# Kernel optimization log

Hardware: AMD Instinct MI355X
Metric: run time of the kernel (lower is better)

The kernel has to match this reference:

```python
import math
import jax, jax.numpy as jnp
import numpy as np

EMB = 1024
HEADS = 16
EXPAND = 2
HEAD_D = EMB // HEADS * EXPAND  # 128
N, S = 2, 2048


def setup_inputs() -> dict:
    key = jax.random.key(0)
    ks = jax.random.split(key, 10)
    lim = 1.0 / math.sqrt(EMB)  # nn.Linear default init range
    inp = {
        "query": jax.random.normal(ks[0], (N, S, EMB), dtype=jnp.float32),
        "key": jax.random.normal(ks[1], (N, S, EMB), dtype=jnp.float32),
        "value": jax.random.normal(ks[2], (N, S, EMB), dtype=jnp.float32),
        "mask": jax.random.randint(ks[3], (1, S, S), 0, 2, dtype=jnp.int32),
        "Wq": jax.random.uniform(ks[4], (EMB * EXPAND, EMB), jnp.float32, -lim, lim),
        "bq": jax.random.uniform(ks[5], (EMB * EXPAND,), jnp.float32, -lim, lim),
        "Wk": jax.random.uniform(ks[6], (EMB * EXPAND, EMB), jnp.float32, -lim, lim),
        "bk": jax.random.uniform(ks[7], (EMB * EXPAND,), jnp.float32, -lim, lim),
        "Wv": jax.random.uniform(ks[8], (EMB * EXPAND, EMB), jnp.float32, -lim, lim),
        "bv": jax.random.uniform(ks[9], (EMB * EXPAND,), jnp.float32, -lim, lim),
    }
    return inp


def _split_heads(x):
    # (N, S, H*D) -> (N, H, S, D)
    n, s, _ = x.shape
    return x.reshape(n, s, HEADS, HEAD_D).transpose(0, 2, 1, 3)


def reference(query, key, value, mask, Wq, bq, Wk, bk, Wv, bv):
    Q = _split_heads(jax.nn.relu(query @ Wq.T + bq))  # (N,H,S,D)
    K = _split_heads(jax.nn.relu(key @ Wk.T + bk))
    V = _split_heads(jax.nn.relu(value @ Wv.T + bv))
    scale = 1.0 / math.sqrt(HEAD_D)
    scores = jnp.einsum("nhqd,nhkd->nhqk", Q, K) * scale  # (N,H,S,S)
    scores = jnp.where(mask[None, :, :, :] == 0, jnp.float32(-1e7), scores)
    probs = jax.nn.softmax(scores, axis=-1)
    y = jnp.einsum("nhqk,nhkd->nhqd", probs, V)  # (N,H,S,D)
    return y.transpose(0, 2, 1, 3).reshape(query.shape[0], S, HEADS * HEAD_D)
```

## Files before the change

### kernel.cpp

```cpp
#include <hip/hip_runtime.h>

typedef __bf16 bf16;
typedef __bf16 bf16x8 __attribute__((ext_vector_type(8)));
typedef __bf16 bf16x4 __attribute__((ext_vector_type(4)));
typedef float f32x4 __attribute__((ext_vector_type(4)));

#define MFMA_BF16(A, B, C) __builtin_amdgcn_mfma_f32_16x16x32_bf16((A), (B), (C), 0, 0, 0)

#define EMB 1024
#define ODIM 2048
#define SEQ 2048
#define HEADS 16
#define HD 128

__global__ __launch_bounds__(256) void build_maskbits_k(const int* __restrict__ mask,
                                                        unsigned long long* __restrict__ mb) {
  int w = blockIdx.x * 256 + threadIdx.x;
  int q = w >> 5, c = w & 31;
  const int4* m4 = reinterpret_cast<const int4*>(mask + (size_t)q * SEQ + c * 64);
  unsigned long long bits = 0ull;
#pragma unroll
  for (int i = 0; i < 16; ++i) {
    int4 v = m4[i];
    if (v.x) bits |= 1ull << (i * 4 + 0);
    if (v.y) bits |= 1ull << (i * 4 + 1);
    if (v.z) bits |= 1ull << (i * 4 + 2);
    if (v.w) bits |= 1ull << (i * 4 + 3);
  }
  mb[w] = bits;
}

__global__ __launch_bounds__(256) void proj_gemm_k(const float* __restrict__ X,
                                                   const float* __restrict__ W,
                                                   const float* __restrict__ bias,
                                                   bf16* __restrict__ outN,
                                                   bf16* __restrict__ outT,
                                                   int vmode, float oscale) {
  __shared__ union {
    struct { bf16 A[128][40]; bf16 B[128][40]; } s;
    bf16 C[128][136];
  } sm;

  const int t = threadIdx.x;
  const int lane = t & 63;
  const int wid = t >> 6;
  const int wm = wid >> 1, wn = wid & 1;
  const int lr = lane & 15, lg = lane >> 4;
  const int m0 = blockIdx.y * 128;
  const int n0 = blockIdx.x * 128;
  const int sr = t >> 1, sh = (t & 1) * 16;

  const f32x4 fzero = {0.f, 0.f, 0.f, 0.f};
  f32x4 acc[4][4];
#pragma unroll
  for (int i = 0; i < 4; ++i)
#pragma unroll
    for (int j = 0; j < 4; ++j) acc[i][j] = fzero;

  const float* Xr = X + (size_t)(m0 + sr) * EMB + sh;
  const float* Wr = W + (size_t)(n0 + sr) * EMB + sh;

  float4 ar[4], br[4];
  {
    const float4* pa = reinterpret_cast<const float4*>(Xr);
    const float4* pb = reinterpret_cast<const float4*>(Wr);
#pragma unroll
    for (int i = 0; i < 4; ++i) { ar[i] = pa[i]; br[i] = pb[i]; }
  }

  for (int k0 = 0; k0 < EMB; k0 += 32) {
    {
      bf16x8 v0, v1, w0, w1;
      v0[0] = (bf16)ar[0].x; v0[1] = (bf16)ar[0].y; v0[2] = (bf16)ar[0].z; v0[3] = (bf16)ar[0].w;
      v0[4] = (bf16)ar[1].x; v0[5] = (bf16)ar[1].y; v0[6] = (bf16)ar[1].z; v0[7] = (bf16)ar[1].w;
      v1[0] = (bf16)ar[2].x; v1[1] = (bf16)ar[2].y; v1[2] = (bf16)ar[2].z; v1[3] = (bf16)ar[2].w;
      v1[4] = (bf16)ar[3].x; v1[5] = (bf16)ar[3].y; v1[6] = (bf16)ar[3].z; v1[7] = (bf16)ar[3].w;
      w0[0] = (bf16)br[0].x; w0[1] = (bf16)br[0].y; w0[2] = (bf16)br[0].z; w0[3] = (bf16)br[0].w;
      w0[4] = (bf16)br[1].x; w0[5] = (bf16)br[1].y; w0[6] = (bf16)br[1].z; w0[7] = (bf16)br[1].w;
      w1[0] = (bf16)br[2].x; w1[1] = (bf16)br[2].y; w1[2] = (bf16)br[2].z; w1[3] = (bf16)br[2].w;
      w1[4] = (bf16)br[3].x; w1[5] = (bf16)br[3].y; w1[6] = (bf16)br[3].z; w1[7] = (bf16)br[3].w;
      *(bf16x8*)&sm.s.A[sr][sh] = v0;
      *(bf16x8*)&sm.s.A[sr][sh + 8] = v1;
      *(bf16x8*)&sm.s.B[sr][sh] = w0;
      *(bf16x8*)&sm.s.B[sr][sh + 8] = w1;
    }
    __syncthreads();
    if (k0 + 32 < EMB) {
      const float4* pa = reinterpret_cast<const float4*>(Xr + k0 + 32);
      const float4* pb = reinterpret_cast<const float4*>(Wr + k0 + 32);
#pragma unroll
      for (int i = 0; i < 4; ++i) { ar[i] = pa[i]; br[i] = pb[i]; }
    }
    bf16x8 af[4], bfr[4];
#pragma unroll
    for (int i = 0; i < 4; ++i) af[i] = *(const bf16x8*)&sm.s.A[wm * 64 + i * 16 + lr][lg * 8];
#pragma unroll
    for (int i = 0; i < 4; ++i) bfr[i] = *(const bf16x8*)&sm.s.B[wn * 64 + i * 16 + lr][lg * 8];
#pragma unroll
    for (int mi = 0; mi < 4; ++mi)
#pragma unroll
      for (int ni = 0; ni < 4; ++ni)
        acc[mi][ni] = MFMA_BF16(af[mi], bfr[ni], acc[mi][ni]);
    __syncthreads();
  }

  float bv_[4];
#pragma unroll
  for (int ni = 0; ni < 4; ++ni) bv_[ni] = bias[n0 + wn * 64 + ni * 16 + lr];

  if (!vmode) {
#pragma unroll
    for (int mi = 0; mi < 4; ++mi)
#pragma unroll
      for (int ni = 0; ni < 4; ++ni)
#pragma unroll
        for (int j = 0; j < 4; ++j) {
          float v = fmaxf(acc[mi][ni][j] + bv_[ni], 0.f) * oscale;
          int row = m0 + wm * 64 + mi * 16 + lg * 4 + j;
          int col = n0 + wn * 64 + ni * 16 + lr;
          outN[(size_t)row * ODIM + col] = (bf16)v;
        }
  } else {
#pragma unroll
    for (int mi = 0; mi < 4; ++mi)
#pragma unroll
      for (int ni = 0; ni < 4; ++ni)
#pragma unroll
        for (int j = 0; j < 4; ++j) {
          float v = fmaxf(acc[mi][ni][j] + bv_[ni], 0.f) * oscale;
          int rit = wm * 64 + mi * 16 + lg * 4 + j;
          int cit = wn * 64 + ni * 16 + lr;
          sm.C[cit][rit] = (bf16)v;
        }
    __syncthreads();
    const int n = m0 >> 11;
    const int s0 = m0 & (SEQ - 1);
    const int h = blockIdx.x;
    bf16* base = outT + ((size_t)(n * HEADS + h) * HD) * SEQ + s0;
#pragma unroll
    for (int i = 0; i < 8; ++i) {
      int cid = i * 256 + t;
      int d = cid >> 4, c = cid & 15;
      *(bf16x8*)(base + (size_t)d * SEQ + c * 8) = *(const bf16x8*)&sm.C[d][c * 8];
    }
  }
}


__device__ __forceinline__ int kswz(int r, int c) {
  int b = (r << 8) | (c << 1);
  b ^= (r & 7) << 4;
  return b >> 1;
}
__device__ __forceinline__ int vswz(int d, int s) {
  int b = (d << 7) | (s << 1);
  b ^= (d & 7) << 4;
  return b >> 1;
}

__global__ __launch_bounds__(256, 2) void attn_k(const bf16* __restrict__ Qb,
                                                 const bf16* __restrict__ Kb,
                                                 const bf16* __restrict__ Vt,
                                                 const unsigned long long* __restrict__ mb,
                                                 float* __restrict__ out) {
  __shared__ bf16 Ks[64 * 128];
  __shared__ bf16 Vs[144 * 64];
  __shared__ bf16 Ps[4][32][72];

  const int t = threadIdx.x;
  const int lane = t & 63;
  const int w = t >> 6;
  const int lr = lane & 15, lg = lane >> 4;

  const int bid = blockIdx.x;
  const int swz = (bid & 7) * 64 + (bid >> 3);
  const int nh = swz >> 4;
  const int qt = swz & 15;
  const int n = nh >> 4, h = nh & 15;
  const int qrow = qt * 128 + w * 32;

  {
    int d = 128 + (t >> 4), s4 = (t & 15) * 4;
    bf16 one = (bf16)1.0f, zero = (bf16)0.0f;
    bf16x4 v = {zero, zero, zero, zero};
    if (d == 128) { v[0] = one; v[1] = one; v[2] = one; v[3] = one; }
    *(bf16x4*)&Vs[vswz(d, s4)] = v;
  }

  bf16x8 qf[2][4];
#pragma unroll
  for (int g = 0; g < 2; ++g) {
    const bf16* qp = Qb + (size_t)(n * SEQ + qrow + g * 16 + lr) * ODIM + h * HD + lg * 8;
#pragma unroll
    for (int ks = 0; ks < 4; ++ks) qf[g][ks] = *(const bf16x8*)(qp + ks * 32);
  }

  const bf16* Kg = Kb + (size_t)(n * SEQ) * ODIM + h * HD;
  const bf16* Vg = Vt + (size_t)nh * HD * SEQ;

  const int rK = t >> 4, cK = t & 15;
  const int dV = t >> 3, cV = t & 7;
  const bf16* kgp = Kg + (size_t)rK * ODIM + cK * 8;
  const bf16* vgp = Vg + (size_t)dV * SEQ + cV * 8;

  bf16x8 kreg[4], vreg[4];
#pragma unroll
  for (int i = 0; i < 4; ++i) kreg[i] = *(const bf16x8*)(kgp + (size_t)i * 16 * ODIM);
#pragma unroll
  for (int i = 0; i < 4; ++i) vreg[i] = *(const bf16x8*)(vgp + (size_t)i * 32 * SEQ);

  f32x4 oacc[2][9];
#pragma unroll
  for (int g = 0; g < 2; ++g)
#pragma unroll
    for (int i = 0; i < 9; ++i) oacc[g][i] = {0.f, 0.f, 0.f, 0.f};
  float mrun[2] = {-3.0e38f, -3.0e38f};

  for (int kt = 0; kt < SEQ / 64; ++kt) {
#pragma unroll
    for (int i = 0; i < 4; ++i) *(bf16x8*)&Ks[kswz(rK + i * 16, cK * 8)] = kreg[i];
#pragma unroll
    for (int i = 0; i < 4; ++i) *(bf16x8*)&Vs[vswz(dV + i * 32, cV * 8)] = vreg[i];
    __syncthreads();

    if (kt + 1 < SEQ / 64) {
      const bf16* kn = kgp + (size_t)(kt + 1) * 64 * ODIM;
      const bf16* vn = vgp + (size_t)(kt + 1) * 64;
#pragma unroll
      for (int i = 0; i < 4; ++i) kreg[i] = *(const bf16x8*)(kn + (size_t)i * 16 * ODIM);
#pragma unroll
      for (int i = 0; i < 4; ++i) vreg[i] = *(const bf16x8*)(vn + (size_t)i * 32 * SEQ);
    }

    unsigned long long mw0 = mb[(size_t)(qrow + lr) * 32 + kt];
    unsigned long long mw1 = mb[(size_t)(qrow + 16 + lr) * 32 + kt];

    f32x4 sacc[2][4];
#pragma unroll
    for (int f = 0; f < 4; ++f)
#pragma unroll
      for (int j = 0; j < 4; ++j) {
        int kk = f * 16 + lg * 4 + j;
        sacc[0][f][j] = ((mw0 >> kk) & 1ull) ? 0.f : -1.0e7f;
        sacc[1][f][j] = ((mw1 >> kk) & 1ull) ? 0.f : -1.0e7f;
      }
#pragma unroll
    for (int f = 0; f < 4; ++f) {
#pragma unroll
      for (int ks = 0; ks < 4; ++ks) {
        bf16x8 kf = *(const bf16x8*)&Ks[kswz(f * 16 + lr, ks * 32 + lg * 8)];
        sacc[0][f] = MFMA_BF16(kf, qf[0][ks], sacc[0][f]);
        sacc[1][f] = MFMA_BF16(kf, qf[1][ks], sacc[1][f]);
      }
    }

    float mt[2] = {-3.0e38f, -3.0e38f};
#pragma unroll
    for (int g = 0; g < 2; ++g) {
#pragma unroll
      for (int f = 0; f < 4; ++f) {
        float a = fmaxf(sacc[g][f][0], sacc[g][f][1]);
        float b = fmaxf(sacc[g][f][2], sacc[g][f][3]);
        mt[g] = fmaxf(mt[g], fmaxf(a, b));
      }
      mt[g] = fmaxf(mt[g], __shfl_xor(mt[g], 16));
      mt[g] = fmaxf(mt[g], __shfl_xor(mt[g], 32));
    }

    if (!__all((mt[0] <= mrun[0] + 8.0f) && (mt[1] <= mrun[1] + 8.0f))) {
#pragma unroll
      for (int g = 0; g < 2; ++g) {
        float mnew = fmaxf(mrun[g], mt[g]);
        float alpha = exp2f(mrun[g] - mnew);
        mrun[g] = mnew;
#pragma unroll
        for (int df = 0; df < 9; ++df)
#pragma unroll
          for (int j = 0; j < 4; ++j) oacc[g][df][j] *= alpha;
      }
    }

#pragma unroll
    for (int g = 0; g < 2; ++g)
#pragma unroll
      for (int f = 0; f < 4; ++f) {
        bf16x4 pw;
#pragma unroll
        for (int j = 0; j < 4; ++j) pw[j] = (bf16)exp2f(sacc[g][f][j] - mrun[g]);
        *(bf16x4*)&Ps[w][g * 16 + lr][f * 16 + lg * 4] = pw;
      }

    bf16x8 pB[2][2];
#pragma unroll
    for (int g = 0; g < 2; ++g)
#pragma unroll
      for (int ks = 0; ks < 2; ++ks)
        pB[g][ks] = *(const bf16x8*)&Ps[w][g * 16 + lr][ks * 32 + lg * 8];

#pragma unroll
    for (int df = 0; df < 9; ++df) {
#pragma unroll
      for (int ks = 0; ks < 2; ++ks) {
        bf16x8 vf = *(const bf16x8*)&Vs[vswz(df * 16 + lr, ks * 32 + lg * 8)];
        oacc[0][df] = MFMA_BF16(vf, pB[0][ks], oacc[0][df]);
        oacc[1][df] = MFMA_BF16(vf, pB[1][ks], oacc[1][df]);
      }
    }
    __syncthreads();
  }

#pragma unroll
  for (int g = 0; g < 2; ++g) {
    float l = __shfl(oacc[g][8][0], lr);
    float inv = 1.0f / l;
    float* obase = out + (size_t)(n * SEQ + qrow + g * 16 + lr) * ODIM + h * HD;
#pragma unroll
    for (int df = 0; df < 8; ++df) {
      f32x4 o;
#pragma unroll
      for (int j = 0; j < 4; ++j) o[j] = oacc[g][df][j] * inv;
      *(f32x4*)(obase + df * 16 + lg * 4) = o;
    }
  }
}

extern "C" void kernel_launch(void* const* d_in, const int* in_sizes, int n_in,
                              void* d_out, int out_size, void* d_ws, size_t ws_size,
                              hipStream_t stream) {
  const float* q   = (const float*)d_in[0];
  const float* k   = (const float*)d_in[1];
  const float* v   = (const float*)d_in[2];
  const int*  mask = (const int*)d_in[3];
  const float* Wq  = (const float*)d_in[4];
  const float* bq  = (const float*)d_in[5];
  const float* Wk  = (const float*)d_in[6];
  const float* bk  = (const float*)d_in[7];
  const float* Wv  = (const float*)d_in[8];
  const float* bv  = (const float*)d_in[9];
  float* out = (float*)d_out;

  char* ws = (char*)d_ws;
  const size_t PLANE = (size_t)4096 * 2048 * sizeof(bf16);
  bf16* Qb = (bf16*)ws;
  bf16* Kb = (bf16*)(ws + PLANE);
  bf16* Vt = (bf16*)(ws + 2 * PLANE);
  unsigned long long* mb = (unsigned long long*)(ws + 3 * PLANE);

  const float qscale = 0.08838834764831845f * 1.4426950408889634f;

  build_maskbits_k<<<256, 256, 0, stream>>>(mask, mb);
  proj_gemm_k<<<dim3(16, 32), 256, 0, stream>>>(q, Wq, bq, Qb, nullptr, 0, qscale);
  proj_gemm_k<<<dim3(16, 32), 256, 0, stream>>>(k, Wk, bk, Kb, nullptr, 0, 1.0f);
  proj_gemm_k<<<dim3(16, 32), 256, 0, stream>>>(v, Wv, bv, nullptr, Vt, 1, 1.0f);
  attn_k<<<512, 256, 0, stream>>>(Qb, Kb, Vt, mb, out);
}
```

Baseline: 224.7 us.

## Pre-convert inputs to bf16, batch projections, double-buffer attention K/V tiles

```diff
diff --git a/kernel.cpp b/kernel.cpp
--- a/kernel.cpp
+++ b/kernel.cpp
@@ -12,6 +12,46 @@
 #define SEQ 2048
 #define HEADS 16
 #define HD 128
+
+__device__ __forceinline__ void gload16(const bf16* g, const bf16* l) {
+  __builtin_amdgcn_global_load_lds(
+      (const __attribute__((address_space(1))) unsigned int*)(const void*)g,
+      (__attribute__((address_space(3))) unsigned int*)(void*)l, 16, 0, 0);
+}
+
+__global__ __launch_bounds__(256) void cvt_bf16_k(const float* __restrict__ q,
+                                                  const float* __restrict__ k,
+                                                  const float* __restrict__ v,
+                                                  const float* __restrict__ Wq,
+                                                  const float* __restrict__ Wk,
+                                                  const float* __restrict__ Wv,
+                                                  bf16* __restrict__ Xall,
+                                                  bf16* __restrict__ Wall) {
+  const unsigned XV = 4096u * 1024u / 8u;
+  const unsigned WV = 2048u * 1024u / 8u;
+  unsigned id = blockIdx.x * 256 + threadIdx.x;
+  const float* src;
+  bf16* dst;
+  size_t off;
+  if (id < 3 * XV) {
+    unsigned p = id / XV;
+    off = (size_t)(id - p * XV) * 8;
+    src = (p == 0) ? q : (p == 1 ? k : v);
+    dst = Xall + (size_t)p * (4096u * 1024u);
+  } else {
+    unsigned id2 = id - 3 * XV;
+    unsigned p = id2 / WV;
+    off = (size_t)(id2 - p * WV) * 8;
+    src = (p == 0) ? Wq : (p == 1 ? Wk : Wv);
+    dst = Wall + (size_t)p * (2048u * 1024u);
+  }
+  float4 a = *(const float4*)(src + off);
+  float4 b = *(const float4*)(src + off + 4);
+  bf16x8 o;
+  o[0] = (bf16)a.x; o[1] = (bf16)a.y; o[2] = (bf16)a.z; o[3] = (bf16)a.w;
+  o[4] = (bf16)b.x; o[5] = (bf16)b.y; o[6] = (bf16)b.z; o[7] = (bf16)b.w;
+  *(bf16x8*)(dst + off) = o;
+}
 
 __global__ __launch_bounds__(256) void build_maskbits_k(const int* __restrict__ mask,
                                                         unsigned long long* __restrict__ mb) {
@@ -30,14 +70,17 @@
   mb[w] = bits;
 }
 
-__global__ __launch_bounds__(256) void proj_gemm_k(const float* __restrict__ X,
-                                                   const float* __restrict__ W,
-                                                   const float* __restrict__ bias,
-                                                   bf16* __restrict__ outN,
-                                                   bf16* __restrict__ outT,
-                                                   int vmode, float oscale) {
+__global__ __launch_bounds__(256) void proj_gemm_k(const bf16* __restrict__ Xall,
+                                                   const bf16* __restrict__ Wall,
+                                                   const float* __restrict__ bq,
+                                                   const float* __restrict__ bk_,
+                                                   const float* __restrict__ bv_,
+                                                   bf16* __restrict__ Qb,
+                                                   bf16* __restrict__ Kb,
+                                                   bf16* __restrict__ Vt,
+                                                   float qscale) {
   __shared__ union {
-    struct { bf16 A[128][40]; bf16 B[128][40]; } s;
+    struct { bf16 A[128 * 64]; bf16 B[128 * 64]; } s;
     bf16 C[128][136];
   } sm;
 
@@ -46,76 +89,73 @@
   const int wid = t >> 6;
   const int wm = wid >> 1, wn = wid & 1;
   const int lr = lane & 15, lg = lane >> 4;
+  const int z = blockIdx.z;
   const int m0 = blockIdx.y * 128;
   const int n0 = blockIdx.x * 128;
-  const int sr = t >> 1, sh = (t & 1) * 16;
-
-  const f32x4 fzero = {0.f, 0.f, 0.f, 0.f};
+  const bf16* X = Xall + (size_t)z * (4096u * 1024u);
+  const bf16* W = Wall + (size_t)z * (2048u * 1024u);
+  const float* bias = (z == 0) ? bq : (z == 1 ? bk_ : bv_);
+  const float oscale = (z == 0) ? qscale : 1.0f;
+
+  const int sr_ = t >> 3;
+  const int scb = (t & 7) * 16;
+
   f32x4 acc[4][4];
 #pragma unroll
   for (int i = 0; i < 4; ++i)
 #pragma unroll
-    for (int j = 0; j < 4; ++j) acc[i][j] = fzero;
-
-  const float* Xr = X + (size_t)(m0 + sr) * EMB + sh;
-  const float* Wr = W + (size_t)(n0 + sr) * EMB + sh;
-
-  float4 ar[4], br[4];
-  {
-    const float4* pa = reinterpret_cast<const float4*>(Xr);
-    const float4* pb = reinterpret_cast<const float4*>(Wr);
-#pragma unroll
-    for (int i = 0; i < 4; ++i) { ar[i] = pa[i]; br[i] = pb[i]; }
-  }
-
-  for (int k0 = 0; k0 < EMB; k0 += 32) {
-    {
-      bf16x8 v0, v1, w0, w1;
-      v0[0] = (bf16)ar[0].x; v0[1] = (bf16)ar[0].y; v0[2] = (bf16)ar[0].z; v0[3] = (bf16)ar[0].w;
-      v0[4] = (bf16)ar[1].x; v0[5] = (bf16)ar[1].y; v0[6] = (bf16)ar[1].z; v0[7] = (bf16)ar[1].w;
-      v1[0] = (bf16)ar[2].x; v1[1] = (bf16)ar[2].y; v1[2] = (bf16)ar[2].z; v1[3] = (bf16)ar[2].w;
-      v1[4] = (bf16)ar[3].x; v1[5] = (bf16)ar[3].y; v1[6] = (bf16)ar[3].z; v1[7] = (bf16)ar[3].w;
-      w0[0] = (bf16)br[0].x; w0[1] = (bf16)br[0].y; w0[2] = (bf16)br[0].z; w0[3] = (bf16)br[0].w;
-      w0[4] = (bf16)br[1].x; w0[5] = (bf16)br[1].y; w0[6] = (bf16)br[1].z; w0[7] = (bf16)br[1].w;
-      w1[0] = (bf16)br[2].x; w1[1] = (bf16)br[2].y; w1[2] = (bf16)br[2].z; w1[3] = (bf16)br[2].w;
-      w1[4] = (bf16)br[3].x; w1[5] = (bf16)br[3].y; w1[6] = (bf16)br[3].z; w1[7] = (bf16)br[3].w;
-      *(bf16x8*)&sm.s.A[sr][sh] = v0;
-      *(bf16x8*)&sm.s.A[sr][sh + 8] = v1;
-      *(bf16x8*)&sm.s.B[sr][sh] = w0;
-      *(bf16x8*)&sm.s.B[sr][sh + 8] = w1;
+    for (int j = 0; j < 4; ++j) acc[i][j] = {0.f, 0.f, 0.f, 0.f};
+
+  for (int k0 = 0; k0 < EMB; k0 += 64) {
+#pragma unroll
+    for (int j = 0; j < 4; ++j) {
+      int r = j * 32 + sr_;
+      int cb = scb ^ ((r & 7) << 4);
+      gload16(X + (size_t)(m0 + r) * EMB + k0 + (cb >> 1), &sm.s.A[j * 2048 + t * 8]);
+    }
+#pragma unroll
+    for (int j = 0; j < 4; ++j) {
+      int r = j * 32 + sr_;
+      int cb = scb ^ ((r & 7) << 4);
+      gload16(W + (size_t)(n0 + r) * EMB + k0 + (cb >> 1), &sm.s.B[j * 2048 + t * 8]);
     }
     __syncthreads();
-    if (k0 + 32 < EMB) {
-      const float4* pa = reinterpret_cast<const float4*>(Xr + k0 + 32);
-      const float4* pb = reinterpret_cast<const float4*>(Wr + k0 + 32);
-#pragma unroll
-      for (int i = 0; i < 4; ++i) { ar[i] = pa[i]; br[i] = pb[i]; }
-    }
-    bf16x8 af[4], bfr[4];
-#pragma unroll
-    for (int i = 0; i < 4; ++i) af[i] = *(const bf16x8*)&sm.s.A[wm * 64 + i * 16 + lr][lg * 8];
-#pragma unroll
-    for (int i = 0; i < 4; ++i) bfr[i] = *(const bf16x8*)&sm.s.B[wn * 64 + i * 16 + lr][lg * 8];
+
+    bf16x8 af[4][2], bfr[4][2];
+#pragma unroll
+    for (int i = 0; i < 4; ++i)
+#pragma unroll
+      for (int s = 0; s < 2; ++s) {
+        int ra = wm * 64 + i * 16 + lr;
+        int ca = (s * 64 + lg * 16) ^ ((ra & 7) << 4);
+        af[i][s] = *(const bf16x8*)&sm.s.A[ra * 64 + (ca >> 1)];
+        int rb = wn * 64 + i * 16 + lr;
+        int cb2 = (s * 64 + lg * 16) ^ ((rb & 7) << 4);
+        bfr[i][s] = *(const bf16x8*)&sm.s.B[rb * 64 + (cb2 >> 1)];
+      }
+#pragma unroll
+    for (int s = 0; s < 2; ++s)
+#pragma unroll
+      for (int mi = 0; mi < 4; ++mi)
+#pragma unroll
+        for (int ni = 0; ni < 4; ++ni)
+          acc[mi][ni] = MFMA_BF16(af[mi][s], bfr[ni][s], acc[mi][ni]);
+    __syncthreads();
+  }
+
+  float bv4[4];
+#pragma unroll
+  for (int ni = 0; ni < 4; ++ni) bv4[ni] = bias[n0 + wn * 64 + ni * 16 + lr];
+
+  if (z < 2) {
+    bf16* outN = (z == 0) ? Qb : Kb;
 #pragma unroll
     for (int mi = 0; mi < 4; ++mi)
 #pragma unroll
       for (int ni = 0; ni < 4; ++ni)
-        acc[mi][ni] = MFMA_BF16(af[mi], bfr[ni], acc[mi][ni]);
-    __syncthreads();
-  }
-
-  float bv_[4];
-#pragma unroll
-  for (int ni = 0; ni < 4; ++ni) bv_[ni] = bias[n0 + wn * 64 + ni * 16 + lr];
-
-  if (!vmode) {
-#pragma unroll
-    for (int mi = 0; mi < 4; ++mi)
-#pragma unroll
-      for (int ni = 0; ni < 4; ++ni)
 #pragma unroll
         for (int j = 0; j < 4; ++j) {
-          float v = fmaxf(acc[mi][ni][j] + bv_[ni], 0.f) * oscale;
+          float v = fmaxf(acc[mi][ni][j] + bv4[ni], 0.f) * oscale;
           int row = m0 + wm * 64 + mi * 16 + lg * 4 + j;
           int col = n0 + wn * 64 + ni * 16 + lr;
           outN[(size_t)row * ODIM + col] = (bf16)v;
@@ -127,7 +167,7 @@
       for (int ni = 0; ni < 4; ++ni)
 #pragma unroll
         for (int j = 0; j < 4; ++j) {
-          float v = fmaxf(acc[mi][ni][j] + bv_[ni], 0.f) * oscale;
+          float v = fmaxf(acc[mi][ni][j] + bv4[ni], 0.f);
           int rit = wm * 64 + mi * 16 + lg * 4 + j;
           int cit = wn * 64 + ni * 16 + lr;
           sm.C[cit][rit] = (bf16)v;
@@ -136,7 +176,7 @@
     const int n = m0 >> 11;
     const int s0 = m0 & (SEQ - 1);
     const int h = blockIdx.x;
-    bf16* base = outT + ((size_t)(n * HEADS + h) * HD) * SEQ + s0;
+    bf16* base = Vt + ((size_t)(n * HEADS + h) * HD) * SEQ + s0;
 #pragma unroll
     for (int i = 0; i < 8; ++i) {
       int cid = i * 256 + t;
@@ -158,14 +198,14 @@
   return b >> 1;
 }
 
-__global__ __launch_bounds__(256, 2) void attn_k(const bf16* __restrict__ Qb,
+__global__ __launch_bounds__(512, 2) void attn_k(const bf16* __restrict__ Qb,
                                                  const bf16* __restrict__ Kb,
                                                  const bf16* __restrict__ Vt,
                                                  const unsigned long long* __restrict__ mb,
                                                  float* __restrict__ out) {
-  __shared__ bf16 Ks[64 * 128];
-  __shared__ bf16 Vs[144 * 64];
-  __shared__ bf16 Ps[4][32][72];
+  __shared__ bf16 Ks[2][64 * 128];
+  __shared__ bf16 Vs[2][128 * 64];
+  __shared__ bf16 Ps[8][32][72];
 
   const int t = threadIdx.x;
   const int lane = t & 63;
@@ -173,19 +213,11 @@
   const int lr = lane & 15, lg = lane >> 4;
 
   const int bid = blockIdx.x;
-  const int swz = (bid & 7) * 64 + (bid >> 3);
-  const int nh = swz >> 4;
-  const int qt = swz & 15;
+  const int swz = (bid & 7) * 32 + (bid >> 3);
+  const int nh = swz >> 3;
+  const int qt = swz & 7;
   const int n = nh >> 4, h = nh & 15;
-  const int qrow = qt * 128 + w * 32;
-
-  {
-    int d = 128 + (t >> 4), s4 = (t & 15) * 4;
-    bf16 one = (bf16)1.0f, zero = (bf16)0.0f;
-    bf16x4 v = {zero, zero, zero, zero};
-    if (d == 128) { v[0] = one; v[1] = one; v[2] = one; v[3] = one; }
-    *(bf16x4*)&Vs[vswz(d, s4)] = v;
-  }
+  const int qrow = qt * 256 + w * 32;
 
   bf16x8 qf[2][4];
 #pragma unroll
@@ -193,6 +225,13 @@
     const bf16* qp = Qb + (size_t)(n * SEQ + qrow + g * 16 + lr) * ODIM + h * HD + lg * 8;
 #pragma unroll
     for (int ks = 0; ks < 4; ++ks) qf[g][ks] = *(const bf16x8*)(qp + ks * 32);
+  }
+
+  bf16x8 onesA;
+  {
+    bf16 o1 = (bf16)((lr == 0) ? 1.0f : 0.0f);
+#pragma unroll
+    for (int j = 0; j < 8; ++j) onesA[j] = o1;
   }
 
   const bf16* Kg = Kb + (size_t)(n * SEQ) * ODIM + h * HD;
@@ -203,11 +242,16 @@
   const bf16* kgp = Kg + (size_t)rK * ODIM + cK * 8;
   const bf16* vgp = Vg + (size_t)dV * SEQ + cV * 8;
 
-  bf16x8 kreg[4], vreg[4];
-#pragma unroll
-  for (int i = 0; i < 4; ++i) kreg[i] = *(const bf16x8*)(kgp + (size_t)i * 16 * ODIM);
-#pragma unroll
-  for (int i = 0; i < 4; ++i) vreg[i] = *(const bf16x8*)(vgp + (size_t)i * 32 * SEQ);
+  bf16x8 kreg[2], vreg[2];
+#pragma unroll
+  for (int i = 0; i < 2; ++i) kreg[i] = *(const bf16x8*)(kgp + (size_t)i * 32 * ODIM);
+#pragma unroll
+  for (int i = 0; i < 2; ++i) vreg[i] = *(const bf16x8*)(vgp + (size_t)i * 64 * SEQ);
+#pragma unroll
+  for (int i = 0; i < 2; ++i) *(bf16x8*)&Ks[0][kswz(rK + i * 32, cK * 8)] = kreg[i];
+#pragma unroll
+  for (int i = 0; i < 2; ++i) *(bf16x8*)&Vs[0][vswz(dV + i * 64, cV * 8)] = vreg[i];
+  __syncthreads();
 
   f32x4 oacc[2][9];
 #pragma unroll
@@ -216,20 +260,17 @@
     for (int i = 0; i < 9; ++i) oacc[g][i] = {0.f, 0.f, 0.f, 0.f};
   float mrun[2] = {-3.0e38f, -3.0e38f};
 
-  for (int kt = 0; kt < SEQ / 64; ++kt) {
-#pragma unroll
-    for (int i = 0; i < 4; ++i) *(bf16x8*)&Ks[kswz(rK + i * 16, cK * 8)] = kreg[i];
-#pragma unroll
-    for (int i = 0; i < 4; ++i) *(bf16x8*)&Vs[vswz(dV + i * 32, cV * 8)] = vreg[i];
-    __syncthreads();
-
-    if (kt + 1 < SEQ / 64) {
+  const int NT = SEQ / 64;
+  for (int kt = 0; kt < NT; ++kt) {
+    const int cur = kt & 1;
+
+    if (kt + 1 < NT) {
       const bf16* kn = kgp + (size_t)(kt + 1) * 64 * ODIM;
       const bf16* vn = vgp + (size_t)(kt + 1) * 64;
 #pragma unroll
-      for (int i = 0; i < 4; ++i) kreg[i] = *(const bf16x8*)(kn + (size_t)i * 16 * ODIM);
-#pragma unroll
-      for (int i = 0; i < 4; ++i) vreg[i] = *(const bf16x8*)(vn + (size_t)i * 32 * SEQ);
+      for (int i = 0; i < 2; ++i) kreg[i] = *(const bf16x8*)(kn + (size_t)i * 32 * ODIM);
+#pragma unroll
+      for (int i = 0; i < 2; ++i) vreg[i] = *(const bf16x8*)(vn + (size_t)i * 64 * SEQ);
     }
 
     unsigned long long mw0 = mb[(size_t)(qrow + lr) * 32 + kt];
@@ -248,7 +289,7 @@
     for (int f = 0; f < 4; ++f) {
 #pragma unroll
       for (int ks = 0; ks < 4; ++ks) {
-        bf16x8 kf = *(const bf16x8*)&Ks[kswz(f * 16 + lr, ks * 32 + lg * 8)];
+        bf16x8 kf = *(const bf16x8*)&Ks[cur][kswz(f * 16 + lr, ks * 32 + lg * 8)];
         sacc[0][f] = MFMA_BF16(kf, qf[0][ks], sacc[0][f]);
         sacc[1][f] = MFMA_BF16(kf, qf[1][ks], sacc[1][f]);
       }
@@ -290,6 +331,13 @@
         *(bf16x4*)&Ps[w][g * 16 + lr][f * 16 + lg * 4] = pw;
       }
 
+    if (kt + 1 < NT) {
+#pragma unroll
+      for (int i = 0; i < 2; ++i) *(bf16x8*)&Ks[cur ^ 1][kswz(rK + i * 32, cK * 8)] = kreg[i];
+#pragma unroll
+      for (int i = 0; i < 2; ++i) *(bf16x8*)&Vs[cur ^ 1][vswz(dV + i * 64, cV * 8)] = vreg[i];
+    }
+
     bf16x8 pB[2][2];
 #pragma unroll
     for (int g = 0; g < 2; ++g)
@@ -298,13 +346,18 @@
         pB[g][ks] = *(const bf16x8*)&Ps[w][g * 16 + lr][ks * 32 + lg * 8];
 
 #pragma unroll
-    for (int df = 0; df < 9; ++df) {
+    for (int df = 0; df < 8; ++df) {
 #pragma unroll
       for (int ks = 0; ks < 2; ++ks) {
-        bf16x8 vf = *(const bf16x8*)&Vs[vswz(df * 16 + lr, ks * 32 + lg * 8)];
+        bf16x8 vf = *(const bf16x8*)&Vs[cur][vswz(df * 16 + lr, ks * 32 + lg * 8)];
         oacc[0][df] = MFMA_BF16(vf, pB[0][ks], oacc[0][df]);
         oacc[1][df] = MFMA_BF16(vf, pB[1][ks], oacc[1][df]);
       }
+    }
+#pragma unroll
+    for (int ks = 0; ks < 2; ++ks) {
+      oacc[0][8] = MFMA_BF16(onesA, pB[0][ks], oacc[0][8]);
+      oacc[1][8] = MFMA_BF16(onesA, pB[1][ks], oacc[1][8]);
     }
     __syncthreads();
   }
@@ -345,12 +398,13 @@
   bf16* Kb = (bf16*)(ws + PLANE);
   bf16* Vt = (bf16*)(ws + 2 * PLANE);
   unsigned long long* mb = (unsigned long long*)(ws + 3 * PLANE);
+  bf16* Xall = (bf16*)(ws + 3 * PLANE + (4u << 20));
+  bf16* Wall = (bf16*)(ws + 3 * PLANE + (4u << 20) + (size_t)3 * 4096 * 1024 * 2);
 
   const float qscale = 0.08838834764831845f * 1.4426950408889634f;
 
+  cvt_bf16_k<<<9216, 256, 0, stream>>>(q, k, v, Wq, Wk, Wv, Xall, Wall);
   build_maskbits_k<<<256, 256, 0, stream>>>(mask, mb);
-  proj_gemm_k<<<dim3(16, 32), 256, 0, stream>>>(q, Wq, bq, Qb, nullptr, 0, qscale);
-  proj_gemm_k<<<dim3(16, 32), 256, 0, stream>>>(k, Wk, bk, Kb, nullptr, 0, 1.0f);
-  proj_gemm_k<<<dim3(16, 32), 256, 0, stream>>>(v, Wv, bv, nullptr, Vt, 1, 1.0f);
-  attn_k<<<512, 256, 0, stream>>>(Qb, Kb, Vt, mb, out);
-}
+  proj_gemm_k<<<dim3(16, 32, 3), 256, 0, stream>>>(Xall, Wall, bq, bk, bv, Qb, Kb, Vt, qscale);
+  attn_k<<<256, 512, 0, stream>>>(Qb, Kb, Vt, mb, out);
+}
```

Result: faster. 198.2 us (-11.8%).
